# Kernel tuning notes

Measured on AMD Instinct MI355X. Metric: run time of the kernel, lower is better.

## Reference

```python
import jax, jax.numpy as jnp
import numpy as np

K = 3
PAD = 1
EPS = 1e-5


def _unfold(x, k, pad):
    # torch.nn.Unfold(k, dilation=1, padding=pad, stride=1): output [B, C*k*k, L]
    # with channel-major ordering (c, ki, kj) in the second dim.
    B, C, H, W = x.shape
    xp = jnp.pad(x, ((0, 0), (0, 0), (pad, pad), (pad, pad)))
    Ho = H + 2 * pad - k + 1
    Wo = W + 2 * pad - k + 1
    patches = jnp.stack(
        [xp[:, :, i:i + Ho, j:j + Wo] for i in range(k) for j in range(k)],
        axis=2,
    )  # [B, C, k*k, Ho, Wo]
    return patches.reshape(B, C * k * k, Ho * Wo)


def _conv1x1(x, w, b):
    return jnp.einsum('bchw,oc->bohw', x, w) + b[None, :, None, None]


def _bn(x, g, b):
    # training-mode BatchNorm2d: batch stats over (B,H,W), biased variance
    mu = x.mean(axis=(0, 2, 3), keepdims=True)
    var = x.var(axis=(0, 2, 3), keepdims=True)
    return (x - mu) * jax.lax.rsqrt(var + EPS) * g[None, :, None, None] + b[None, :, None, None]


def _tri(x, w, b, g, be):
    return jax.nn.relu(_bn(_conv1x1(x, w, b), g, be))


def reference(x, w1, b1, g1, be1, w2, b2, g2, be2, wf, bf, gf, bef):
    B, C, H, W = x.shape
    k2 = K * K
    c = k2 // 2
    tri1 = _tri(x, w1, b1, g1, be1)  # key map  [B,C,H,W] (m=1)
    tri2 = _tri(x, w2, b2, g2, be2)  # query map
    # NOTE: faithful to source: plain row-major reshape of [B, C*k2, L] -> [B, C, L, k2]
    ku = _unfold(tri1, K, PAD).reshape(B, C, -1, k2)
    qu = _unfold(tri2, K, PAD).reshape(B, C, -1, k2)
    logits = ku * qu[..., c:c + 1] + ku[..., c:c + 1] * qu
    dl_weight = jax.nn.softmax(logits, axis=-1)[:, None]  # [B,1,C,L,k2]
    xu = _unfold(x, K, PAD).reshape(B, 1, C, -1, k2)       # m=1 -> [B,1,C,L,k2]
    # NOTE: faithful to source: row-major reshape to [B, C, k2, L], sum over axis -2
    pre = (dl_weight * xu).reshape(B, C, k2, -1).sum(axis=-2).reshape(B, C, H, W)
    return jax.nn.relu(_bn(_conv1x1(pre, wf, bf), gf, bef))


def setup_inputs() -> dict:
    key = jax.random.key(0)
    B, C, O, H, W = 4, 256, 256, 64, 64
    ks = jax.random.split(key, 4)
    s = 1.0 / np.sqrt(C)
    return {
        'x': jax.random.normal(ks[0], (B, C, H, W), dtype=jnp.float32),
        'w1': jax.random.normal(ks[1], (C, C), dtype=jnp.float32) * s,
        'b1': jnp.zeros((C,), jnp.float32),
        'g1': jnp.ones((C,), jnp.float32),
        'be1': jnp.zeros((C,), jnp.float32),
        'w2': jax.random.normal(ks[2], (C, C), dtype=jnp.float32) * s,
        'b2': jnp.zeros((C,), jnp.float32),
        'g2': jnp.ones((C,), jnp.float32),
        'be2': jnp.zeros((C,), jnp.float32),
        'wf': jax.random.normal(ks[3], (O, C), dtype=jnp.float32) * s,
        'bf': jnp.zeros((O,), jnp.float32),
        'gf': jnp.ones((O,), jnp.float32),
        'bef': jnp.zeros((O,), jnp.float32),
    }
```

## Files before the change

kernel.cpp:

```cpp
#include <hip/hip_runtime.h>
#include <hip/hip_bf16.h>

#define L 4096
#define CCH 256
#define NB 4
#define KP 40
#define GOF 72
#define LOG2E 1.4426950408889634f
#define INVN (1.0f / (NB * (float)L))
#define NPART 256

typedef __attribute__((ext_vector_type(8))) short short8;
typedef __attribute__((ext_vector_type(4))) float f32x4;
typedef unsigned short ushort_t;

__device__ __forceinline__ unsigned short f2bf(float f) {
    unsigned u = __builtin_bit_cast(unsigned, f);
    u += 0x7FFF + ((u >> 16) & 1);
    return (unsigned short)(u >> 16);
}
__device__ __forceinline__ unsigned pk_bf16(float a, float b) {
    __hip_bfloat162 h = __float22bfloat162_rn(make_float2(a, b));
    unsigned u;
    __builtin_memcpy(&u, &h, 4);
    return u;
}
__device__ __forceinline__ float bflo(unsigned w) {
    return __builtin_bit_cast(float, w << 16);
}
__device__ __forceinline__ float bfhi(unsigned w) {
    return __builtin_bit_cast(float, w & 0xFFFF0000u);
}
__device__ __forceinline__ float bfu(ushort_t h) {
    return __builtin_bit_cast(float, (unsigned)h << 16);
}

__global__ __launch_bounds__(256) void wcvt_k(
    const float* __restrict__ w1, const float* __restrict__ w2,
    const float* __restrict__ wf,
    ushort_t* __restrict__ wb1, ushort_t* __restrict__ wb2,
    ushort_t* __restrict__ wbf)
{
    const int mb = blockIdx.x >> 6;
    const int i  = (blockIdx.x & 63) * 256 + threadIdx.x;
    const float* src = (mb == 0) ? w1 : (mb == 1) ? w2 : wf;
    ushort_t*    dst = (mb == 0) ? wb1 : (mb == 1) ? wb2 : wbf;
    float4 v = ((const float4*)src)[i];
    uint2 p;
    p.x = pk_bf16(v.x, v.y);
    p.y = pk_bf16(v.z, v.w);
    ((uint2*)dst)[i] = p;
}

__global__ __launch_bounds__(256, 3) void dual_gemm_k(
    const float* __restrict__ x,
    const ushort_t* __restrict__ wb1, const float* __restrict__ b1,
    const ushort_t* __restrict__ wb2, const float* __restrict__ b2,
    ushort_t* __restrict__ y1, ushort_t* __restrict__ y2,
    float* __restrict__ stPS1, float* __restrict__ stPQ1,
    float* __restrict__ stPS2, float* __restrict__ stPQ2)
{
    __shared__ short sA1[2][128 * KP];
    __shared__ short sA2[2][128 * KP];
    __shared__ short sB [2][64 * KP];

    const int tid = threadIdx.x;
    const int l0 = blockIdx.x * 64;
    const int o0 = blockIdx.y * 128;
    const int b  = blockIdx.z;
    const int part = b * 64 + blockIdx.x;

    const int wv = tid >> 6;
    const int lane = tid & 63;
    const int m = lane & 15;
    const int quad = lane >> 4;

    const float* xb = x + (size_t)b * CCH * L;

    const int sl = tid & 63, soct = tid >> 6;
    const int sr = tid & 127, sh = tid >> 7;

    f32x4 acc1[2][4], acc2[2][4];
    #pragma unroll
    for (int io = 0; io < 2; ++io)
        #pragma unroll
        for (int jl = 0; jl < 4; ++jl) {
            acc1[io][jl] = (f32x4){0.f,0.f,0.f,0.f};
            acc2[io][jl] = (f32x4){0.f,0.f,0.f,0.f};
        }

    float fx[8];
    uint4 pw1a, pw1b, pw2a, pw2b;

    auto LOADT = [&](int s) {
        const int k0 = s * 32;
        const float* xs = xb + (size_t)(k0 + soct * 8) * L + l0 + sl;
        #pragma unroll
        for (int j = 0; j < 8; ++j) fx[j] = xs[(size_t)j * L];
        const uint4* wp = (const uint4*)&wb1[(size_t)(o0 + sr) * CCH + k0 + sh * 16];
        pw1a = wp[0]; pw1b = wp[1];
        const uint4* wq = (const uint4*)&wb2[(size_t)(o0 + sr) * CCH + k0 + sh * 16];
        pw2a = wq[0]; pw2b = wq[1];
    };
    auto STORET = [&](int buf) {
        uint4 v;
        v.x = pk_bf16(fx[0], fx[1]);
        v.y = pk_bf16(fx[2], fx[3]);
        v.z = pk_bf16(fx[4], fx[5]);
        v.w = pk_bf16(fx[6], fx[7]);
        *(uint4*)&sB[buf][sl * KP + soct * 8] = v;
        *(uint4*)&sA1[buf][sr * KP + sh * 16]     = pw1a;
        *(uint4*)&sA1[buf][sr * KP + sh * 16 + 8] = pw1b;
        *(uint4*)&sA2[buf][sr * KP + sh * 16]     = pw2a;
        *(uint4*)&sA2[buf][sr * KP + sh * 16 + 8] = pw2b;
    };

    LOADT(0);
    STORET(0);
    __syncthreads();

    for (int s = 0; s < 8; ++s) {
        const int buf = s & 1;
        if (s < 7) LOADT(s + 1);

        short8 a1[2], a2[2], bfr[4];
        #pragma unroll
        for (int io = 0; io < 2; ++io) {
            a1[io] = *(const short8*)&sA1[buf][(wv * 32 + io * 16 + m) * KP + quad * 8];
            a2[io] = *(const short8*)&sA2[buf][(wv * 32 + io * 16 + m) * KP + quad * 8];
        }
        #pragma unroll
        for (int jl = 0; jl < 4; ++jl)
            bfr[jl] = *(const short8*)&sB[buf][(jl * 16 + m) * KP + quad * 8];
        #pragma unroll
        for (int io = 0; io < 2; ++io)
            #pragma unroll
            for (int jl = 0; jl < 4; ++jl) {
                acc1[io][jl] = __builtin_amdgcn_mfma_f32_16x16x32_bf16(a1[io], bfr[jl], acc1[io][jl], 0, 0, 0);
                acc2[io][jl] = __builtin_amdgcn_mfma_f32_16x16x32_bf16(a2[io], bfr[jl], acc2[io][jl], 0, 0, 0);
            }

        if (s < 7) STORET(buf ^ 1);
        __syncthreads();
    }

    #pragma unroll
    for (int io = 0; io < 2; ++io)
        #pragma unroll
        for (int reg = 0; reg < 4; ++reg) {
            const int o = o0 + wv * 32 + io * 16 + quad * 4 + reg;
            const float bb1 = b1[o], bb2 = b2[o];
            float v1[4], v2[4];
            #pragma unroll
            for (int jl = 0; jl < 4; ++jl) {
                v1[jl] = acc1[io][jl][reg] + bb1;
                v2[jl] = acc2[io][jl][reg] + bb2;
            }
            const size_t ro = ((size_t)b * CCH + o) * L + l0 + m;
            unsigned u1a = pk_bf16(v1[0], v1[1]);
            unsigned u1b = pk_bf16(v1[2], v1[3]);
            unsigned u2a = pk_bf16(v2[0], v2[1]);
            unsigned u2b = pk_bf16(v2[2], v2[3]);
            y1[ro]      = (ushort_t)u1a;
            y1[ro + 16] = (ushort_t)(u1a >> 16);
            y1[ro + 32] = (ushort_t)u1b;
            y1[ro + 48] = (ushort_t)(u1b >> 16);
            y2[ro]      = (ushort_t)u2a;
            y2[ro + 16] = (ushort_t)(u2a >> 16);
            y2[ro + 32] = (ushort_t)u2b;
            y2[ro + 48] = (ushort_t)(u2b >> 16);

            float s1 = (v1[0] + v1[1]) + (v1[2] + v1[3]);
            float q1 = (v1[0]*v1[0] + v1[1]*v1[1]) + (v1[2]*v1[2] + v1[3]*v1[3]);
            float s2 = (v2[0] + v2[1]) + (v2[2] + v2[3]);
            float q2 = (v2[0]*v2[0] + v2[1]*v2[1]) + (v2[2]*v2[2] + v2[3]*v2[3]);
            #pragma unroll
            for (int d = 1; d < 16; d <<= 1) {
                s1 += __shfl_xor(s1, d); q1 += __shfl_xor(q1, d);
                s2 += __shfl_xor(s2, d); q2 += __shfl_xor(q2, d);
            }
            if (m == 0) {
                stPS1[o * NPART + part] = s1; stPQ1[o * NPART + part] = q1;
                stPS2[o * NPART + part] = s2; stPQ2[o * NPART + part] = q2;
            }
        }
}

__global__ __launch_bounds__(256, 4) void single_gemm_k(
    const ushort_t* __restrict__ x,
    const ushort_t* __restrict__ wb, const float* __restrict__ bb,
    ushort_t* __restrict__ y,
    float* __restrict__ stPS, float* __restrict__ stPQ)
{
    __shared__ short sA[2][128 * KP];
    __shared__ short sB[2][64 * KP];

    const int tid = threadIdx.x;
    const int l0 = blockIdx.x * 64;
    const int o0 = blockIdx.y * 128;
    const int b  = blockIdx.z;
    const int part = b * 64 + blockIdx.x;

    const int wv = tid >> 6;
    const int lane = tid & 63;
    const int m = lane & 15;
    const int quad = lane >> 4;

    const ushort_t* xb = x + (size_t)b * CCH * L;

    const int sl = tid & 63, soct = tid >> 6;
    const int sr = tid & 127, sh = tid >> 7;

    f32x4 acc[2][4];
    #pragma unroll
    for (int io = 0; io < 2; ++io)
        #pragma unroll
        for (int jl = 0; jl < 4; ++jl)
            acc[io][jl] = (f32x4){0.f,0.f,0.f,0.f};

    ushort_t hx[8];
    uint4 pwa, pwb;

    auto LOADT = [&](int s) {
        const int k0 = s * 32;
        const ushort_t* xs = xb + (size_t)(k0 + soct * 8) * L + l0 + sl;
        #pragma unroll
        for (int j = 0; j < 8; ++j) hx[j] = xs[(size_t)j * L];
        const uint4* wp = (const uint4*)&wb[(size_t)(o0 + sr) * CCH + k0 + sh * 16];
        pwa = wp[0]; pwb = wp[1];
    };
    auto STORET = [&](int buf) {
        short8 v;
        #pragma unroll
        for (int j = 0; j < 8; ++j) v[j] = (short)hx[j];
        *(short8*)&sB[buf][sl * KP + soct * 8] = v;
        *(uint4*)&sA[buf][sr * KP + sh * 16]     = pwa;
        *(uint4*)&sA[buf][sr * KP + sh * 16 + 8] = pwb;
    };

    LOADT(0);
    STORET(0);
    __syncthreads();

    for (int s = 0; s < 8; ++s) {
        const int buf = s & 1;
        if (s < 7) LOADT(s + 1);

        short8 a[2], bfr[4];
        #pragma unroll
        for (int io = 0; io < 2; ++io)
            a[io] = *(const short8*)&sA[buf][(wv * 32 + io * 16 + m) * KP + quad * 8];
        #pragma unroll
        for (int jl = 0; jl < 4; ++jl)
            bfr[jl] = *(const short8*)&sB[buf][(jl * 16 + m) * KP + quad * 8];
        #pragma unroll
        for (int io = 0; io < 2; ++io)
            #pragma unroll
            for (int jl = 0; jl < 4; ++jl)
                acc[io][jl] = __builtin_amdgcn_mfma_f32_16x16x32_bf16(a[io], bfr[jl], acc[io][jl], 0, 0, 0);

        if (s < 7) STORET(buf ^ 1);
        __syncthreads();
    }

    #pragma unroll
    for (int io = 0; io < 2; ++io)
        #pragma unroll
        for (int reg = 0; reg < 4; ++reg) {
            const int o = o0 + wv * 32 + io * 16 + quad * 4 + reg;
            const float b0 = bb[o];
            float v[4];
            #pragma unroll
            for (int jl = 0; jl < 4; ++jl) v[jl] = acc[io][jl][reg] + b0;
            const size_t ro = ((size_t)b * CCH + o) * L + l0 + m;
            unsigned ua = pk_bf16(v[0], v[1]);
            unsigned ub = pk_bf16(v[2], v[3]);
            y[ro]      = (ushort_t)ua;
            y[ro + 16] = (ushort_t)(ua >> 16);
            y[ro + 32] = (ushort_t)ub;
            y[ro + 48] = (ushort_t)(ub >> 16);

            float s0 = (v[0] + v[1]) + (v[2] + v[3]);
            float q0 = (v[0]*v[0] + v[1]*v[1]) + (v[2]*v[2] + v[3]*v[3]);
            #pragma unroll
            for (int d = 1; d < 16; d <<= 1) {
                s0 += __shfl_xor(s0, d); q0 += __shfl_xor(q0, d);
            }
            if (m == 0) {
                stPS[o * NPART + part] = s0; stPQ[o * NPART + part] = q0;
            }
        }
}

__global__ __launch_bounds__(512, 6) void attention_k(
    const float* __restrict__ x,
    const ushort_t* __restrict__ y1,
    const ushort_t* __restrict__ y2,
    const float* __restrict__ stPS1, const float* __restrict__ stPQ1,
    const float* __restrict__ stPS2, const float* __restrict__ stPQ2,
    const float* __restrict__ g1, const float* __restrict__ be1,
    const float* __restrict__ g2, const float* __restrict__ be2,
    ushort_t* __restrict__ pre)
{
    __shared__ unsigned sKQg[4240];
    __shared__ ushort_t sXg [4240];
    __shared__ float    accF[L];
    __shared__ float    redS[8], redQ[8], bnP[4];

    const int bc = blockIdx.x;
    const int tid = threadIdx.x;
    const int ch = bc & 255;
    const size_t off = (size_t)bc * L;
    const int wid = tid >> 6, lane = tid & 63;

    {
        const float* PS = (tid < 256) ? stPS1 : stPS2;
        const float* PQ = (tid < 256) ? stPQ1 : stPQ2;
        const int t = tid & 255;
        float s = PS[ch * NPART + t];
        float q = PQ[ch * NPART + t];
        #pragma unroll
        for (int d = 1; d < 64; d <<= 1) {
            s += __shfl_xor(s, d);
            q += __shfl_xor(q, d);
        }
        if (lane == 0) { redS[wid] = s; redQ[wid] = q; }
    }
    if (tid < GOF)  { sKQg[tid] = 0; sXg[tid] = 0; }
    if (tid < 72)   { sKQg[GOF + 4096 + tid] = 0; sXg[GOF + 4096 + tid] = 0; }
    {
        float4 z = {0.f, 0.f, 0.f, 0.f};
        ((float4*)accF)[tid]       = z;
        ((float4*)accF)[tid + 512] = z;
    }
    __syncthreads();
    if (tid == 0) {
        float S1 = (redS[0] + redS[1]) + (redS[2] + redS[3]);
        float Q1 = (redQ[0] + redQ[1]) + (redQ[2] + redQ[3]);
        float S2 = (redS[4] + redS[5]) + (redS[6] + redS[7]);
        float Q2 = (redQ[4] + redQ[5]) + (redQ[6] + redQ[7]);
        float mean = S1 * INVN, var = Q1 * INVN - mean * mean;
        float rstd = rsqrtf(var + 1e-5f);
        float g = g1[ch];
        bnP[0] = LOG2E * g * rstd;
        bnP[1] = LOG2E * (be1[ch] - mean * g * rstd);
        mean = S2 * INVN; var = Q2 * INVN - mean * mean;
        rstd = rsqrtf(var + 1e-5f);
        g = g2[ch];
        bnP[2] = g * rstd;
        bnP[3] = be2[ch] - mean * g * rstd;
    }
    __syncthreads();
    const float sc1 = bnP[0], sh1 = bnP[1];
    const float sc2 = bnP[2], sh2 = bnP[3];

    {
        uint4 ak = ((const uint4*)(y1 + off))[tid];
        uint4 aq = ((const uint4*)(y2 + off))[tid];
        float4 xa = ((const float4*)(x + off))[2 * tid];
        float4 xb = ((const float4*)(x + off))[2 * tid + 1];
        unsigned wk[4] = {ak.x, ak.y, ak.z, ak.w};
        unsigned wq[4] = {aq.x, aq.y, aq.z, aq.w};
        unsigned kq[8];
        #pragma unroll
        for (int u = 0; u < 4; ++u) {
            float klo = fmaxf(fmaf(bflo(wk[u]), sc1, sh1), 0.f);
            float khi = fmaxf(fmaf(bfhi(wk[u]), sc1, sh1), 0.f);
            float qlo = fmaxf(fmaf(bflo(wq[u]), sc2, sh2), 0.f);
            float qhi = fmaxf(fmaf(bfhi(wq[u]), sc2, sh2), 0.f);
            kq[2*u]   = (unsigned)f2bf(klo) | ((unsigned)f2bf(qlo) << 16);
            kq[2*u+1] = (unsigned)f2bf(khi) | ((unsigned)f2bf(qhi) << 16);
        }
        *(uint4*)&sKQg[GOF + 8 * tid]     = make_uint4(kq[0], kq[1], kq[2], kq[3]);
        *(uint4*)&sKQg[GOF + 8 * tid + 4] = make_uint4(kq[4], kq[5], kq[6], kq[7]);
        float xv[8] = {xa.x, xa.y, xa.z, xa.w, xb.x, xb.y, xb.z, xb.w};
        unsigned xp[4];
        #pragma unroll
        for (int u = 0; u < 4; ++u)
            xp[u] = (unsigned)f2bf(xv[2*u]) | ((unsigned)f2bf(xv[2*u+1]) << 16);
        *(uint4*)&sXg[GOF + 8 * tid] = make_uint4(xp[0], xp[1], xp[2], xp[3]);
    }
    __syncthreads();

    {
        const int fbase = 9 * tid;
        #pragma unroll
        for (int r = 0; r < 8; ++r) {
            const int f  = fbase + 4608 * r;
            const int t  = f >> 12;
            const int fl = f & 4095;
            unsigned wv[9];
            float    xw[9];
            const bool fastp = (fl < 4088);
            if (fastp) {
                const int di = (t * 86) >> 8;
                const int dj = t - 3 * di;
                const int cbad = (dj == 0) ? 0 : ((dj == 2) ? 63 : 99);
                const int base = fl + (di << 6) + dj - 65 + GOF;
                #pragma unroll
                for (int j = 0; j < 9; ++j) {
                    wv[j] = sKQg[base + j];
                    xw[j] = bfu(sXg[base + j]);
                }
                #pragma unroll
                for (int j = 0; j < 9; ++j) {
                    int c = (fl + j) & 63;
                    bool bad = (c == cbad);
                    wv[j] = bad ? 0u  : wv[j];
                    xw[j] = bad ? 0.f : xw[j];
                }
            } else {
                #pragma unroll
                for (int j = 0; j < 9; ++j) {
                    int fj = f + j;
                    int tj = fj >> 12, lj = fj & 4095;
                    int dij = (tj * 86) >> 8, djj = tj - 3 * dij;
                    int idx = lj + (dij << 6) + djj - 65 + GOF;
                    unsigned wr = sKQg[idx];
                    float    xr = bfu(sXg[idx]);
                    int c = lj & 63;
                    int cb = (djj == 0) ? 0 : ((djj == 2) ? 63 : 99);
                    bool bad = (c == cb);
                    wv[j] = bad ? 0u  : wr;
                    xw[j] = bad ? 0.f : xr;
                }
            }
            const unsigned cw = wv[4];
            const float kc = bflo(cw), qc = bfhi(cw);
            float e[9];
            #pragma unroll
            for (int j = 0; j < 9; ++j)
                e[j] = __builtin_amdgcn_exp2f(bflo(wv[j]) * qc + kc * bfhi(wv[j]));
            float s = (((e[0] + e[1]) + (e[2] + e[3])) +
                       ((e[4] + e[5]) + (e[6] + e[7]))) + e[8];
            const float rinv = __builtin_amdgcn_rcpf(s);
            float cj[9];
            #pragma unroll
            for (int j = 0; j < 9; ++j)
                cj[j] = e[j] * rinv * xw[j];

            __syncthreads();
            if (tid < 455) {
                if (fastp) {
                    #pragma unroll
                    for (int j = 0; j < 9; ++j) accF[fl + j] += cj[j];
                } else {
                    #pragma unroll
                    for (int j = 0; j < 9; ++j) accF[(f + j) & 4095] += cj[j];
                }
            }
            __syncthreads();
            if (tid >= 455) {
                if (fastp) {
                    #pragma unroll
                    for (int j = 0; j < 9; ++j) accF[fl + j] += cj[j];
                } else {
                    #pragma unroll
                    for (int j = 0; j < 9; ++j) accF[(f + j) & 4095] += cj[j];
                }
            }
        }
    }
    __syncthreads();

    {
        unsigned* po = (unsigned*)(pre + off);
        #pragma unroll
        for (int rr = 0; rr < 4; ++rr) {
            const int p = rr * 512 + tid;
            po[p] = pk_bf16(accF[2 * p], accF[2 * p + 1]);
        }
    }
}

__global__ __launch_bounds__(256) void bn_apply_k(
    const ushort_t* __restrict__ yf,
    const float* __restrict__ stPS, const float* __restrict__ stPQ,
    const float* __restrict__ gf, const float* __restrict__ bef,
    float* __restrict__ out)
{
    __shared__ float redS[4], redQ[4], bnP[2];

    const int c = blockIdx.x & 255;
    const int b = blockIdx.x >> 8;
    const int tid = threadIdx.x;
    const int wid = tid >> 6, lane = tid & 63;

    {
        float s = stPS[c * NPART + tid];
        float q = stPQ[c * NPART + tid];
        #pragma unroll
        for (int d = 1; d < 64; d <<= 1) {
            s += __shfl_xor(s, d);
            q += __shfl_xor(q, d);
        }
        if (lane == 0) { redS[wid] = s; redQ[wid] = q; }
    }
    __syncthreads();
    if (tid == 0) {
        float S = (redS[0] + redS[1]) + (redS[2] + redS[3]);
        float Q = (redQ[0] + redQ[1]) + (redQ[2] + redQ[3]);
        float mean = S * INVN, var = Q * INVN - mean * mean;
        float rstd = rsqrtf(var + 1e-5f);
        float g = gf[c];
        bnP[0] = g * rstd;
        bnP[1] = bef[c] - mean * g * rstd;
    }
    __syncthreads();
    const float sc = bnP[0], sh = bnP[1];

    const uint4* p = (const uint4*)(yf + ((size_t)b * CCH + c) * L);
    float4* o = (float4*)(out + ((size_t)b * CCH + c) * L);
    #pragma unroll
    for (int r = 0; r < 2; ++r) {
        uint4 v = p[r * 256 + tid];
        unsigned w[4] = {v.x, v.y, v.z, v.w};
        float4 o0, o1;
        o0.x = fmaxf(fmaf(bflo(w[0]), sc, sh), 0.f);
        o0.y = fmaxf(fmaf(bfhi(w[0]), sc, sh), 0.f);
        o0.z = fmaxf(fmaf(bflo(w[1]), sc, sh), 0.f);
        o0.w = fmaxf(fmaf(bfhi(w[1]), sc, sh), 0.f);
        o1.x = fmaxf(fmaf(bflo(w[2]), sc, sh), 0.f);
        o1.y = fmaxf(fmaf(bfhi(w[2]), sc, sh), 0.f);
        o1.z = fmaxf(fmaf(bflo(w[3]), sc, sh), 0.f);
        o1.w = fmaxf(fmaf(bfhi(w[3]), sc, sh), 0.f);
        int i = r * 256 + tid;
        o[2 * i]     = o0;
        o[2 * i + 1] = o1;
    }
}

extern "C" void kernel_launch(void* const* d_in, const int* in_sizes, int n_in,
                              void* d_out, int out_size, void* d_ws, size_t ws_size,
                              hipStream_t stream) {
    const float* x   = (const float*)d_in[0];
    const float* w1  = (const float*)d_in[1];
    const float* b1  = (const float*)d_in[2];
    const float* g1  = (const float*)d_in[3];
    const float* be1 = (const float*)d_in[4];
    const float* w2  = (const float*)d_in[5];
    const float* b2  = (const float*)d_in[6];
    const float* g2  = (const float*)d_in[7];
    const float* be2 = (const float*)d_in[8];
    const float* wf  = (const float*)d_in[9];
    const float* bf  = (const float*)d_in[10];
    const float* gf  = (const float*)d_in[11];
    const float* bef = (const float*)d_in[12];
    float* out = (float*)d_out;

    const size_t NEL = (size_t)NB * CCH * L;
    const size_t PSZ = (size_t)CCH * NPART;
    ushort_t* y1b = (ushort_t*)d_ws;
    ushort_t* y2b = y1b + NEL;
    float* stP = (float*)(y2b + NEL);
    float* stPS1 = stP,            *stPQ1 = stP + PSZ;
    float* stPS2 = stP + 2 * PSZ,  *stPQ2 = stP + 3 * PSZ;
    float* stPSF = stP + 4 * PSZ,  *stPQF = stP + 5 * PSZ;
    ushort_t* wb1 = (ushort_t*)(stP + 6 * PSZ);
    ushort_t* wb2 = wb1 + CCH * CCH;
    ushort_t* wbf = wb2 + CCH * CCH;

    wcvt_k<<<192, 256, 0, stream>>>(w1, w2, wf, wb1, wb2, wbf);
    dim3 gg(64, 2, 4);
    dual_gemm_k<<<gg, 256, 0, stream>>>(x, wb1, b1, wb2, b2, y1b, y2b,
                                        stPS1, stPQ1, stPS2, stPQ2);
    attention_k<<<NB * CCH, 512, 0, stream>>>(x, y1b, y2b,
                                              stPS1, stPQ1, stPS2, stPQ2,
                                              g1, be1, g2, be2,
                                              y2b);
    single_gemm_k<<<gg, 256, 0, stream>>>(y2b, wbf, bf, y1b,
                                          stPSF, stPQF);
    bn_apply_k<<<NB * CCH, 256, 0, stream>>>(y1b, stPSF, stPQF, gf, bef, out);
}
```

Before: 163.0 us.

## Fuse weight bf16 conversion into GEMM loads and interleave K/Q/X smem

Removes the separate weight-conversion kernel: both GEMM kernels now read fp32 weights directly and pack them to bf16 while staging into shared memory. That saves one launch and a round trip through global memory, but doubles the weight bytes loaded per tile and adds conversion work and registers inside the GEMMs. In the attention kernel, the separate packed key/query array and bf16 x array in shared memory are merged into one interleaved uint2 array. Each neighbour tap then needs a single 8-byte LDS read instead of two, at the cost of more shared memory (the x value now sits in a 32-bit slot).

```diff
diff --git a/kernel.cpp b/kernel.cpp
--- a/kernel.cpp
+++ b/kernel.cpp
@@ -35,27 +35,10 @@
     return __builtin_bit_cast(float, (unsigned)h << 16);
 }
 
-__global__ __launch_bounds__(256) void wcvt_k(
-    const float* __restrict__ w1, const float* __restrict__ w2,
-    const float* __restrict__ wf,
-    ushort_t* __restrict__ wb1, ushort_t* __restrict__ wb2,
-    ushort_t* __restrict__ wbf)
-{
-    const int mb = blockIdx.x >> 6;
-    const int i  = (blockIdx.x & 63) * 256 + threadIdx.x;
-    const float* src = (mb == 0) ? w1 : (mb == 1) ? w2 : wf;
-    ushort_t*    dst = (mb == 0) ? wb1 : (mb == 1) ? wb2 : wbf;
-    float4 v = ((const float4*)src)[i];
-    uint2 p;
-    p.x = pk_bf16(v.x, v.y);
-    p.y = pk_bf16(v.z, v.w);
-    ((uint2*)dst)[i] = p;
-}
-
 __global__ __launch_bounds__(256, 3) void dual_gemm_k(
     const float* __restrict__ x,
-    const ushort_t* __restrict__ wb1, const float* __restrict__ b1,
-    const ushort_t* __restrict__ wb2, const float* __restrict__ b2,
+    const float* __restrict__ w1, const float* __restrict__ b1,
+    const float* __restrict__ w2, const float* __restrict__ b2,
     ushort_t* __restrict__ y1, ushort_t* __restrict__ y2,
     float* __restrict__ stPS1, float* __restrict__ stPQ1,
     float* __restrict__ stPS2, float* __restrict__ stPQ2)
@@ -90,17 +73,19 @@
         }
 
     float fx[8];
-    uint4 pw1a, pw1b, pw2a, pw2b;
+    float4 w1r[4], w2r[4];
 
     auto LOADT = [&](int s) {
         const int k0 = s * 32;
         const float* xs = xb + (size_t)(k0 + soct * 8) * L + l0 + sl;
         #pragma unroll
         for (int j = 0; j < 8; ++j) fx[j] = xs[(size_t)j * L];
-        const uint4* wp = (const uint4*)&wb1[(size_t)(o0 + sr) * CCH + k0 + sh * 16];
-        pw1a = wp[0]; pw1b = wp[1];
-        const uint4* wq = (const uint4*)&wb2[(size_t)(o0 + sr) * CCH + k0 + sh * 16];
-        pw2a = wq[0]; pw2b = wq[1];
+        const float4* wp = (const float4*)&w1[(size_t)(o0 + sr) * CCH + k0 + sh * 16];
+        #pragma unroll
+        for (int j = 0; j < 4; ++j) w1r[j] = wp[j];
+        const float4* wq = (const float4*)&w2[(size_t)(o0 + sr) * CCH + k0 + sh * 16];
+        #pragma unroll
+        for (int j = 0; j < 4; ++j) w2r[j] = wq[j];
     };
     auto STORET = [&](int buf) {
         uint4 v;
@@ -109,10 +94,20 @@
         v.z = pk_bf16(fx[4], fx[5]);
         v.w = pk_bf16(fx[6], fx[7]);
         *(uint4*)&sB[buf][sl * KP + soct * 8] = v;
-        *(uint4*)&sA1[buf][sr * KP + sh * 16]     = pw1a;
-        *(uint4*)&sA1[buf][sr * KP + sh * 16 + 8] = pw1b;
-        *(uint4*)&sA2[buf][sr * KP + sh * 16]     = pw2a;
-        *(uint4*)&sA2[buf][sr * KP + sh * 16 + 8] = pw2b;
+        uint4 a0, a1;
+        a0.x = pk_bf16(w1r[0].x, w1r[0].y); a0.y = pk_bf16(w1r[0].z, w1r[0].w);
+        a0.z = pk_bf16(w1r[1].x, w1r[1].y); a0.w = pk_bf16(w1r[1].z, w1r[1].w);
+        a1.x = pk_bf16(w1r[2].x, w1r[2].y); a1.y = pk_bf16(w1r[2].z, w1r[2].w);
+        a1.z = pk_bf16(w1r[3].x, w1r[3].y); a1.w = pk_bf16(w1r[3].z, w1r[3].w);
+        *(uint4*)&sA1[buf][sr * KP + sh * 16]     = a0;
+        *(uint4*)&sA1[buf][sr * KP + sh * 16 + 8] = a1;
+        uint4 c0, c1;
+        c0.x = pk_bf16(w2r[0].x, w2r[0].y); c0.y = pk_bf16(w2r[0].z, w2r[0].w);
+        c0.z = pk_bf16(w2r[1].x, w2r[1].y); c0.w = pk_bf16(w2r[1].z, w2r[1].w);
+        c1.x = pk_bf16(w2r[2].x, w2r[2].y); c1.y = pk_bf16(w2r[2].z, w2r[2].w);
+        c1.z = pk_bf16(w2r[3].x, w2r[3].y); c1.w = pk_bf16(w2r[3].z, w2r[3].w);
+        *(uint4*)&sA2[buf][sr * KP + sh * 16]     = c0;
+        *(uint4*)&sA2[buf][sr * KP + sh * 16 + 8] = c1;
     };
 
     LOADT(0);
@@ -188,7 +183,7 @@
 
 __global__ __launch_bounds__(256, 4) void single_gemm_k(
     const ushort_t* __restrict__ x,
-    const ushort_t* __restrict__ wb, const float* __restrict__ bb,
+    const float* __restrict__ wf, const float* __restrict__ bb,
     ushort_t* __restrict__ y,
     float* __restrict__ stPS, float* __restrict__ stPQ)
 {
@@ -219,23 +214,29 @@
             acc[io][jl] = (f32x4){0.f,0.f,0.f,0.f};
 
     ushort_t hx[8];
-    uint4 pwa, pwb;
+    float4 wr[4];
 
     auto LOADT = [&](int s) {
         const int k0 = s * 32;
         const ushort_t* xs = xb + (size_t)(k0 + soct * 8) * L + l0 + sl;
         #pragma unroll
         for (int j = 0; j < 8; ++j) hx[j] = xs[(size_t)j * L];
-        const uint4* wp = (const uint4*)&wb[(size_t)(o0 + sr) * CCH + k0 + sh * 16];
-        pwa = wp[0]; pwb = wp[1];
+        const float4* wp = (const float4*)&wf[(size_t)(o0 + sr) * CCH + k0 + sh * 16];
+        #pragma unroll
+        for (int j = 0; j < 4; ++j) wr[j] = wp[j];
     };
     auto STORET = [&](int buf) {
         short8 v;
         #pragma unroll
         for (int j = 0; j < 8; ++j) v[j] = (short)hx[j];
         *(short8*)&sB[buf][sl * KP + soct * 8] = v;
-        *(uint4*)&sA[buf][sr * KP + sh * 16]     = pwa;
-        *(uint4*)&sA[buf][sr * KP + sh * 16 + 8] = pwb;
+        uint4 a0, a1;
+        a0.x = pk_bf16(wr[0].x, wr[0].y); a0.y = pk_bf16(wr[0].z, wr[0].w);
+        a0.z = pk_bf16(wr[1].x, wr[1].y); a0.w = pk_bf16(wr[1].z, wr[1].w);
+        a1.x = pk_bf16(wr[2].x, wr[2].y); a1.y = pk_bf16(wr[2].z, wr[2].w);
+        a1.z = pk_bf16(wr[3].x, wr[3].y); a1.w = pk_bf16(wr[3].z, wr[3].w);
+        *(uint4*)&sA[buf][sr * KP + sh * 16]     = a0;
+        *(uint4*)&sA[buf][sr * KP + sh * 16 + 8] = a1;
     };
 
     LOADT(0);
@@ -302,10 +303,9 @@
     const float* __restrict__ g2, const float* __restrict__ be2,
     ushort_t* __restrict__ pre)
 {
-    __shared__ unsigned sKQg[4240];
-    __shared__ ushort_t sXg [4240];
-    __shared__ float    accF[L];
-    __shared__ float    redS[8], redQ[8], bnP[4];
+    __shared__ uint2 sKQX[4240];
+    __shared__ float accF[L];
+    __shared__ float redS[8], redQ[8], bnP[4];
 
     const int bc = blockIdx.x;
     const int tid = threadIdx.x;
@@ -326,8 +326,8 @@
         }
         if (lane == 0) { redS[wid] = s; redQ[wid] = q; }
     }
-    if (tid < GOF)  { sKQg[tid] = 0; sXg[tid] = 0; }
-    if (tid < 72)   { sKQg[GOF + 4096 + tid] = 0; sXg[GOF + 4096 + tid] = 0; }
+    if (tid < GOF)  sKQX[tid] = make_uint2(0u, 0u);
+    if (tid < 72)   sKQX[GOF + 4096 + tid] = make_uint2(0u, 0u);
     {
         float4 z = {0.f, 0.f, 0.f, 0.f};
         ((float4*)accF)[tid]       = z;
@@ -361,6 +361,7 @@
         float4 xb = ((const float4*)(x + off))[2 * tid + 1];
         unsigned wk[4] = {ak.x, ak.y, ak.z, ak.w};
         unsigned wq[4] = {aq.x, aq.y, aq.z, aq.w};
+        float xv[8] = {xa.x, xa.y, xa.z, xa.w, xb.x, xb.y, xb.z, xb.w};
         unsigned kq[8];
         #pragma unroll
         for (int u = 0; u < 4; ++u) {
@@ -371,14 +372,14 @@
             kq[2*u]   = (unsigned)f2bf(klo) | ((unsigned)f2bf(qlo) << 16);
             kq[2*u+1] = (unsigned)f2bf(khi) | ((unsigned)f2bf(qhi) << 16);
         }
-        *(uint4*)&sKQg[GOF + 8 * tid]     = make_uint4(kq[0], kq[1], kq[2], kq[3]);
-        *(uint4*)&sKQg[GOF + 8 * tid + 4] = make_uint4(kq[4], kq[5], kq[6], kq[7]);
-        float xv[8] = {xa.x, xa.y, xa.z, xa.w, xb.x, xb.y, xb.z, xb.w};
-        unsigned xp[4];
-        #pragma unroll
-        for (int u = 0; u < 4; ++u)
-            xp[u] = (unsigned)f2bf(xv[2*u]) | ((unsigned)f2bf(xv[2*u+1]) << 16);
-        *(uint4*)&sXg[GOF + 8 * tid] = make_uint4(xp[0], xp[1], xp[2], xp[3]);
+        unsigned xp[8];
+        #pragma unroll
+        for (int e = 0; e < 8; ++e) xp[e] = (unsigned)f2bf(xv[e]);
+        uint2* dst = &sKQX[GOF + 8 * tid];
+        *(uint4*)&dst[0] = make_uint4(kq[0], xp[0], kq[1], xp[1]);
+        *(uint4*)&dst[2] = make_uint4(kq[2], xp[2], kq[3], xp[3]);
+        *(uint4*)&dst[4] = make_uint4(kq[4], xp[4], kq[5], xp[5]);
+        *(uint4*)&dst[6] = make_uint4(kq[6], xp[6], kq[7], xp[7]);
     }
     __syncthreads();
 
@@ -399,8 +400,9 @@
                 const int base = fl + (di << 6) + dj - 65 + GOF;
                 #pragma unroll
                 for (int j = 0; j < 9; ++j) {
-                    wv[j] = sKQg[base + j];
-                    xw[j] = bfu(sXg[base + j]);
+                    uint2 v = sKQX[base + j];
+                    wv[j] = v.x;
+                    xw[j] = bfu((ushort_t)v.y);
                 }
                 #pragma unroll
                 for (int j = 0; j < 9; ++j) {
@@ -416,13 +418,12 @@
                     int tj = fj >> 12, lj = fj & 4095;
                     int dij = (tj * 86) >> 8, djj = tj - 3 * dij;
                     int idx = lj + (dij << 6) + djj - 65 + GOF;
-                    unsigned wr = sKQg[idx];
-                    float    xr = bfu(sXg[idx]);
+                    uint2 v = sKQX[idx];
                     int c = lj & 63;
                     int cb = (djj == 0) ? 0 : ((djj == 2) ? 63 : 99);
                     bool bad = (c == cb);
-                    wv[j] = bad ? 0u  : wr;
-                    xw[j] = bad ? 0.f : xr;
+                    wv[j] = bad ? 0u  : v.x;
+                    xw[j] = bad ? 0.f : bfu((ushort_t)v.y);
                 }
             }
             const unsigned cw = wv[4];
@@ -556,19 +557,15 @@
     float* stPS1 = stP,            *stPQ1 = stP + PSZ;
     float* stPS2 = stP + 2 * PSZ,  *stPQ2 = stP + 3 * PSZ;
     float* stPSF = stP + 4 * PSZ,  *stPQF = stP + 5 * PSZ;
-    ushort_t* wb1 = (ushort_t*)(stP + 6 * PSZ);
-    ushort_t* wb2 = wb1 + CCH * CCH;
-    ushort_t* wbf = wb2 + CCH * CCH;
-
-    wcvt_k<<<192, 256, 0, stream>>>(w1, w2, wf, wb1, wb2, wbf);
+
     dim3 gg(64, 2, 4);
-    dual_gemm_k<<<gg, 256, 0, stream>>>(x, wb1, b1, wb2, b2, y1b, y2b,
+    dual_gemm_k<<<gg, 256, 0, stream>>>(x, w1, b1, w2, b2, y1b, y2b,
                                         stPS1, stPQ1, stPS2, stPQ2);
     attention_k<<<NB * CCH, 512, 0, stream>>>(x, y1b, y2b,
                                               stPS1, stPQ1, stPS2, stPQ2,
                                               g1, be1, g2, be2,
                                               y2b);
-    single_gemm_k<<<gg, 256, 0, stream>>>(y2b, wbf, bf, y1b,
+    single_gemm_k<<<gg, 256, 0, stream>>>(y2b, wf, bf, y1b,
                                           stPSF, stPQF);
     bn_apply_k<<<NB * CCH, 256, 0, stream>>>(y1b, stPSF, stPQF, gf, bef, out);
 }
```

Result: slower. 171.6 us (+5.3%).
